# Performance work log

Measured on AMD Instinct MI355X. Metric: run time of the kernel, lower is better.

Reference implementation:

```python
import jax, jax.numpy as jnp
import numpy as np

N, E, IN, HID, H, G, OUT = 50000, 800000, 128, 96, 8, 64, 10
D = HID // H  # per-head dim = 12


def setup_inputs() -> dict:
    key = jax.random.key(0)
    ks = jax.random.split(key, 24)
    s = 0.1
    inp = {
        'x': jax.random.normal(ks[0], (N, IN), jnp.float32),
        'src': jax.random.randint(ks[1], (E,), 0, N, jnp.int32),
        'dst': jax.random.randint(ks[2], (E,), 0, N, jnp.int32),
        'graph_id': jax.random.randint(ks[3], (N,), 0, G, jnp.int32),
        # GraphConv layers (norm='both', weight + bias)
        'W1': jax.random.normal(ks[4], (IN, HID), jnp.float32) * s,
        'b1': jnp.zeros((HID,), jnp.float32),
        'W2': jax.random.normal(ks[5], (HID, HID), jnp.float32) * s,
        'b2': jnp.zeros((HID,), jnp.float32),
        # 3 GATv2 layers, stacked params
        'Ws': jax.random.normal(ks[6], (3, HID, HID), jnp.float32) * s,
        'bs': jnp.zeros((3, HID), jnp.float32),
        'Wd': jax.random.normal(ks[7], (3, HID, HID), jnp.float32) * s,
        'bd': jnp.zeros((3, HID), jnp.float32),
        'attn': jax.random.normal(ks[8], (3, H, D), jnp.float32) * s,
        # classifier MLP (dropout is identity at inference)
        'Wc1': jax.random.normal(ks[9], (HID, HID), jnp.float32) * s,
        'bc1': jnp.zeros((HID,), jnp.float32),
        'Wc2': jax.random.normal(ks[10], (HID, HID // 2), jnp.float32) * s,
        'bc2': jnp.zeros((HID // 2,), jnp.float32),
        'Wc3': jax.random.normal(ks[11], (HID // 2, OUT), jnp.float32) * s,
        'bc3': jnp.zeros((OUT,), jnp.float32),
    }
    return inp


def _graph_conv(h, W, b, src, dst):
    # DGL GraphConv, norm='both', allow_zero_in_degree (degrees clamped to >=1)
    ones = jnp.ones((E,), h.dtype)
    deg_out = jnp.clip(jax.ops.segment_sum(ones, src, N), 1.0)
    deg_in = jnp.clip(jax.ops.segment_sum(ones, dst, N), 1.0)
    h = (h * (deg_out ** -0.5)[:, None]) @ W          # [N, out]
    agg = jax.ops.segment_sum(h[src], dst, N)          # sum over in-edges
    return agg * (deg_in ** -0.5)[:, None] + b


def _gatv2(h, Ws, bs, Wd, bd, attn, src, dst):
    fs = (h @ Ws + bs).reshape(N, H, D)
    fd = (h @ Wd + bd).reshape(N, H, D)
    e = jax.nn.leaky_relu(fs[src] + fd[dst], 0.2)      # [E, H, D]
    logits = jnp.einsum('ehd,hd->eh', e, attn)         # [E, H]
    # edge softmax over incoming edges of each dst node
    m = jax.ops.segment_max(logits, dst, N)            # [N, H]
    ex = jnp.exp(logits - m[dst])
    den = jax.ops.segment_sum(ex, dst, N)              # [N, H]
    a = ex / den[dst]                                  # [E, H]
    rst = jax.ops.segment_sum(a[:, :, None] * fs[src], dst, N)  # [N, H, D]
    return jax.nn.relu(rst).reshape(N, HID)            # activation=relu, then view


def reference(x, src, dst, graph_id, W1, b1, W2, b2, Ws, bs, Wd, bd, attn,
              Wc1, bc1, Wc2, bc2, Wc3, bc3):
    h = jax.nn.relu(_graph_conv(x, W1, b1, src, dst))
    h = jax.nn.relu(_graph_conv(h, W2, b2, src, dst))
    for i in range(3):
        h = _gatv2(h, Ws[i], bs[i], Wd[i], bd[i], attn[i], src, dst)
    # dgl.max_nodes: per-graph max readout
    hg = jax.ops.segment_max(h, graph_id, G)           # [G, HID]
    z = jax.nn.relu(hg @ Wc1 + bc1)
    z = jax.nn.relu(z @ Wc2 + bc2)
    return z @ Wc3 + bc3                               # [G, OUT]
```

## Files before the change

### kernel.cpp

```cpp
#include <hip/hip_runtime.h>
#include <hip/hip_bf16.h>

#define Nn 50000
#define Ee 800000
#define INF_ 128
#define HIDF 96
#define HH 8
#define DD 12
#define GG 64
#define OUTF 10

#define SCAN_CHUNK 512
#define SCAN_BLOCKS ((Nn + SCAN_CHUNK - 1) / SCAN_CHUNK)
#define RB 128

__global__ void hist_kernel(const int* __restrict__ src, const int* __restrict__ dst,
                            int* cnt_out, int* cnt_in, int* __restrict__ edge_slot, int E) {
    int e = blockIdx.x * 256 + threadIdx.x;
    if (e < E) {
        atomicAdd(&cnt_out[src[e]], 1);
        edge_slot[e] = atomicAdd(&cnt_in[dst[e]], 1);
    }
}

__global__ __launch_bounds__(256) void scan1_kernel(const int* __restrict__ cnt_in,
                                                    int* __restrict__ row_start,
                                                    int* __restrict__ blk_sum, int N) {
    __shared__ int part[256];
    int t = threadIdx.x;
    int base = blockIdx.x * SCAN_CHUNK;
    int i0 = base + 2 * t, i1 = i0 + 1;
    int a = (i0 < N) ? cnt_in[i0] : 0;
    int b = (i1 < N) ? cnt_in[i1] : 0;
    int s = a + b;
    part[t] = s;
    __syncthreads();
    for (int off = 1; off < 256; off <<= 1) {
        int v = (t >= off) ? part[t - off] : 0;
        __syncthreads();
        part[t] += v;
        __syncthreads();
    }
    int excl = part[t] - s;
    if (i0 < N) row_start[i0] = excl;
    if (i1 < N) row_start[i1] = excl + a;
    if (t == 255) blk_sum[blockIdx.x] = part[255];
}

__global__ __launch_bounds__(128) void scan2_kernel(const int* __restrict__ blk_sum,
                                                    int* __restrict__ blk_off,
                                                    int* __restrict__ row_start, int N) {
    __shared__ int part[128];
    int t = threadIdx.x;
    int v0 = (t < SCAN_BLOCKS) ? blk_sum[t] : 0;
    part[t] = v0;
    __syncthreads();
    for (int off = 1; off < 128; off <<= 1) {
        int v = (t >= off) ? part[t - off] : 0;
        __syncthreads();
        part[t] += v;
        __syncthreads();
    }
    blk_off[t] = part[t] - v0;
    if (t == 127) row_start[N] = part[127];
}

__global__ __launch_bounds__(256) void scan3_kernel(int* __restrict__ row_start,
                                                    const int* __restrict__ blk_off, int N) {
    int t = threadIdx.x;
    int base = blockIdx.x * SCAN_CHUNK;
    int off = blk_off[blockIdx.x];
    int i0 = base + 2 * t, i1 = i0 + 1;
    if (i0 < N) row_start[i0] += off;
    if (i1 < N) row_start[i1] += off;
}

__global__ void node_setup(const int* __restrict__ cnt_in, const int* __restrict__ cnt_out,
                           float* __restrict__ degI_is, float* __restrict__ degO_is, int N) {
    int n = blockIdx.x * 256 + threadIdx.x;
    if (n < N) {
        degI_is[n] = rsqrtf((float)max(cnt_in[n], 1));
        degO_is[n] = rsqrtf((float)max(cnt_out[n], 1));
    }
}

__global__ void fill_kernel(const int* __restrict__ src, const int* __restrict__ dst,
                            const int* __restrict__ row_start, const int* __restrict__ edge_slot,
                            int* __restrict__ csr_src, int E) {
    int e = blockIdx.x * 256 + threadIdx.x;
    if (e < E) {
        csr_src[row_start[dst[e]] + edge_slot[e]] = src[e];
    }
}

__global__ __launch_bounds__(192) void gemm96(const float* __restrict__ A, int K,
                                              const float* __restrict__ W,
                                              const float* __restrict__ bias,
                                              const float* __restrict__ rowScale,
                                              float* __restrict__ out, int N) {
    __shared__ float A_lds[64 * 36];
    __shared__ float W_lds[32 * 96];
    const int t = threadIdx.x;
    const int row0 = blockIdx.x * 64;
    const int tcol = t % 24;
    const int trow = t / 24;
    float acc[8][4];
#pragma unroll
    for (int i = 0; i < 8; ++i)
#pragma unroll
        for (int j = 0; j < 4; ++j) acc[i][j] = 0.f;

    for (int k0 = 0; k0 < K; k0 += 32) {
        for (int i = t; i < 32 * 24; i += 192) {
            ((float4*)W_lds)[i] = ((const float4*)W)[(size_t)k0 * 24 + i];
        }
        for (int i = t; i < 64 * 8; i += 192) {
            int r = i / 8, kk = i % 8;
            int gr = row0 + r;
            float4 v = make_float4(0.f, 0.f, 0.f, 0.f);
            if (gr < N) {
                v = *((const float4*)(A + (size_t)gr * K + k0 + kk * 4));
                if (rowScale) {
                    float s = rowScale[gr];
                    v.x *= s; v.y *= s; v.z *= s; v.w *= s;
                }
            }
            *((float4*)(A_lds + r * 36 + kk * 4)) = v;
        }
        __syncthreads();
#pragma unroll
        for (int kk4 = 0; kk4 < 8; ++kk4) {
            float4 a[8];
#pragma unroll
            for (int i = 0; i < 8; ++i)
                a[i] = *((const float4*)(A_lds + (trow + 8 * i) * 36 + kk4 * 4));
#pragma unroll
            for (int kk = 0; kk < 4; ++kk) {
                float4 wv = *((const float4*)(W_lds + (kk4 * 4 + kk) * 96 + tcol * 4));
#pragma unroll
                for (int i = 0; i < 8; ++i) {
                    float av = (kk == 0) ? a[i].x : (kk == 1) ? a[i].y : (kk == 2) ? a[i].z : a[i].w;
                    acc[i][0] = fmaf(av, wv.x, acc[i][0]);
                    acc[i][1] = fmaf(av, wv.y, acc[i][1]);
                    acc[i][2] = fmaf(av, wv.z, acc[i][2]);
                    acc[i][3] = fmaf(av, wv.w, acc[i][3]);
                }
            }
        }
        __syncthreads();
    }
    float4 b4 = bias ? *((const float4*)(bias + tcol * 4)) : make_float4(0.f, 0.f, 0.f, 0.f);
#pragma unroll
    for (int i = 0; i < 8; ++i) {
        int gr = row0 + trow + 8 * i;
        if (gr < N) {
            float4 o = make_float4(acc[i][0] + b4.x, acc[i][1] + b4.y,
                                   acc[i][2] + b4.z, acc[i][3] + b4.w);
            *((float4*)(out + (size_t)gr * 96 + tcol * 4)) = o;
        }
    }
}

__global__ __launch_bounds__(192) void gemm96x2(const float* __restrict__ A,
                                                const float* __restrict__ W1_, const float* __restrict__ b1_,
                                                const float* __restrict__ W2_, const float* __restrict__ b2_,
                                                float* __restrict__ out1, float* __restrict__ out2, int N) {
    __shared__ float A_lds[64 * 36];
    __shared__ float W_lds[2 * 32 * 96];
    const int t = threadIdx.x;
    const int row0 = blockIdx.x * 64;
    const int tcol = t % 24;
    const int trow = t / 24;
    float acc1[8][4], acc2[8][4];
#pragma unroll
    for (int i = 0; i < 8; ++i)
#pragma unroll
        for (int j = 0; j < 4; ++j) { acc1[i][j] = 0.f; acc2[i][j] = 0.f; }

    for (int k0 = 0; k0 < 96; k0 += 32) {
        for (int i = t; i < 32 * 24; i += 192) {
            ((float4*)W_lds)[i] = ((const float4*)W1_)[(size_t)k0 * 24 + i];
            ((float4*)(W_lds + 32 * 96))[i] = ((const float4*)W2_)[(size_t)k0 * 24 + i];
        }
        for (int i = t; i < 64 * 8; i += 192) {
            int r = i / 8, kk = i % 8;
            int gr = row0 + r;
            float4 v = make_float4(0.f, 0.f, 0.f, 0.f);
            if (gr < N) v = *((const float4*)(A + (size_t)gr * 96 + k0 + kk * 4));
            *((float4*)(A_lds + r * 36 + kk * 4)) = v;
        }
        __syncthreads();
#pragma unroll
        for (int kk4 = 0; kk4 < 8; ++kk4) {
            float4 a[8];
#pragma unroll
            for (int i = 0; i < 8; ++i)
                a[i] = *((const float4*)(A_lds + (trow + 8 * i) * 36 + kk4 * 4));
#pragma unroll
            for (int kk = 0; kk < 4; ++kk) {
                float4 wv1 = *((const float4*)(W_lds + (kk4 * 4 + kk) * 96 + tcol * 4));
                float4 wv2 = *((const float4*)(W_lds + 32 * 96 + (kk4 * 4 + kk) * 96 + tcol * 4));
#pragma unroll
                for (int i = 0; i < 8; ++i) {
                    float av = (kk == 0) ? a[i].x : (kk == 1) ? a[i].y : (kk == 2) ? a[i].z : a[i].w;
                    acc1[i][0] = fmaf(av, wv1.x, acc1[i][0]);
                    acc1[i][1] = fmaf(av, wv1.y, acc1[i][1]);
                    acc1[i][2] = fmaf(av, wv1.z, acc1[i][2]);
                    acc1[i][3] = fmaf(av, wv1.w, acc1[i][3]);
                    acc2[i][0] = fmaf(av, wv2.x, acc2[i][0]);
                    acc2[i][1] = fmaf(av, wv2.y, acc2[i][1]);
                    acc2[i][2] = fmaf(av, wv2.z, acc2[i][2]);
                    acc2[i][3] = fmaf(av, wv2.w, acc2[i][3]);
                }
            }
        }
        __syncthreads();
    }
    float4 bb1 = *((const float4*)(b1_ + tcol * 4));
    float4 bb2 = *((const float4*)(b2_ + tcol * 4));
#pragma unroll
    for (int i = 0; i < 8; ++i) {
        int gr = row0 + trow + 8 * i;
        if (gr < N) {
            float4 o1 = make_float4(acc1[i][0] + bb1.x, acc1[i][1] + bb1.y,
                                    acc1[i][2] + bb1.z, acc1[i][3] + bb1.w);
            float4 o2 = make_float4(acc2[i][0] + bb2.x, acc2[i][1] + bb2.y,
                                    acc2[i][2] + bb2.z, acc2[i][3] + bb2.w);
            *((float4*)(out1 + (size_t)gr * 96 + tcol * 4)) = o1;
            *((float4*)(out2 + (size_t)gr * 96 + tcol * 4)) = o2;
        }
    }
}

__global__ __launch_bounds__(192) void gc_agg(const float* __restrict__ hW,
                                              const int* __restrict__ row_start,
                                              const int* __restrict__ csr_src,
                                              const float* __restrict__ degI_is,
                                              const float* __restrict__ bias,
                                              float* __restrict__ hout, int N) {
    int tid = blockIdx.x * 192 + threadIdx.x;
    int n = tid / 24;
    int c = (tid % 24) * 4;
    if (n >= N) return;
    int beg = row_start[n], end = row_start[n + 1];
    float4 s = make_float4(0.f, 0.f, 0.f, 0.f);
    int e = beg;
    for (; e + 4 <= end; e += 4) {
        int i0 = csr_src[e], i1 = csr_src[e + 1], i2 = csr_src[e + 2], i3 = csr_src[e + 3];
        float4 v0 = *(const float4*)(hW + (size_t)i0 * 96 + c);
        float4 v1 = *(const float4*)(hW + (size_t)i1 * 96 + c);
        float4 v2 = *(const float4*)(hW + (size_t)i2 * 96 + c);
        float4 v3 = *(const float4*)(hW + (size_t)i3 * 96 + c);
        s.x += (v0.x + v1.x) + (v2.x + v3.x);
        s.y += (v0.y + v1.y) + (v2.y + v3.y);
        s.z += (v0.z + v1.z) + (v2.z + v3.z);
        s.w += (v0.w + v1.w) + (v2.w + v3.w);
    }
    for (; e < end; ++e) {
        int i0 = csr_src[e];
        float4 v0 = *(const float4*)(hW + (size_t)i0 * 96 + c);
        s.x += v0.x; s.y += v0.y; s.z += v0.z; s.w += v0.w;
    }
    float dn = degI_is[n];
    float4 b = *(const float4*)(bias + c);
    float4 o;
    o.x = fmaxf(fmaf(s.x, dn, b.x), 0.f);
    o.y = fmaxf(fmaf(s.y, dn, b.y), 0.f);
    o.z = fmaxf(fmaf(s.z, dn, b.z), 0.f);
    o.w = fmaxf(fmaf(s.w, dn, b.w), 0.f);
    *(float4*)(hout + (size_t)n * 96 + c) = o;
}

__global__ __launch_bounds__(256) void gat_agg(const float* __restrict__ fs,
                                               const float* __restrict__ fd,
                                               const float* __restrict__ attn,
                                               const int* __restrict__ row_start,
                                               const int* __restrict__ csr_src,
                                               float* __restrict__ hout, int N) {
    int tid = blockIdx.x * 256 + threadIdx.x;
    int n = tid >> 3, hd = tid & 7;
    if (n >= N) return;
    float att[12], fdv[12];
    {
        const float4* ap = (const float4*)(attn + hd * 12);
        float4 a0 = ap[0], a1 = ap[1], a2 = ap[2];
        att[0]=a0.x; att[1]=a0.y; att[2]=a0.z; att[3]=a0.w;
        att[4]=a1.x; att[5]=a1.y; att[6]=a1.z; att[7]=a1.w;
        att[8]=a2.x; att[9]=a2.y; att[10]=a2.z; att[11]=a2.w;
        const float4* dp = (const float4*)(fd + (size_t)n * 96 + hd * 12);
        float4 d0 = dp[0], d1 = dp[1], d2 = dp[2];
        fdv[0]=d0.x; fdv[1]=d0.y; fdv[2]=d0.z; fdv[3]=d0.w;
        fdv[4]=d1.x; fdv[5]=d1.y; fdv[6]=d1.z; fdv[7]=d1.w;
        fdv[8]=d2.x; fdv[9]=d2.y; fdv[10]=d2.z; fdv[11]=d2.w;
    }
    int beg = row_start[n], end = row_start[n + 1];
    float m = -3.0e38f, den = 0.f;
    float acc[12];
#pragma unroll
    for (int d = 0; d < 12; ++d) acc[d] = 0.f;

    auto process = [&](const float4& s0, const float4& s1, const float4& s2) {
        float fsv[12];
        fsv[0]=s0.x; fsv[1]=s0.y; fsv[2]=s0.z; fsv[3]=s0.w;
        fsv[4]=s1.x; fsv[5]=s1.y; fsv[6]=s1.z; fsv[7]=s1.w;
        fsv[8]=s2.x; fsv[9]=s2.y; fsv[10]=s2.z; fsv[11]=s2.w;
        float logit = 0.f;
#pragma unroll
        for (int d = 0; d < 12; ++d) {
            float u = fsv[d] + fdv[d];
            u = u > 0.f ? u : 0.2f * u;
            logit = fmaf(u, att[d], logit);
        }
        float nm = fmaxf(m, logit);
        float cc = __expf(m - nm);
        float w  = __expf(logit - nm);
        den = fmaf(den, cc, w);
#pragma unroll
        for (int d = 0; d < 12; ++d) acc[d] = fmaf(acc[d], cc, w * fsv[d]);
        m = nm;
    };

    int e = beg;
    for (; e + 4 <= end; e += 4) {
        int i0 = csr_src[e], i1 = csr_src[e + 1], i2 = csr_src[e + 2], i3 = csr_src[e + 3];
        const float4* p0 = (const float4*)(fs + (size_t)i0 * 96 + hd * 12);
        const float4* p1 = (const float4*)(fs + (size_t)i1 * 96 + hd * 12);
        const float4* p2 = (const float4*)(fs + (size_t)i2 * 96 + hd * 12);
        const float4* p3 = (const float4*)(fs + (size_t)i3 * 96 + hd * 12);
        float4 a0 = p0[0], a1 = p0[1], a2 = p0[2];
        float4 b0 = p1[0], b1 = p1[1], b2 = p1[2];
        float4 c0 = p2[0], c1 = p2[1], c2 = p2[2];
        float4 d0 = p3[0], d1 = p3[1], d2 = p3[2];
        process(a0, a1, a2);
        process(b0, b1, b2);
        process(c0, c1, c2);
        process(d0, d1, d2);
    }
    for (; e < end; ++e) {
        int i0 = csr_src[e];
        const float4* p0 = (const float4*)(fs + (size_t)i0 * 96 + hd * 12);
        float4 a0 = p0[0], a1 = p0[1], a2 = p0[2];
        process(a0, a1, a2);
    }
    float inv = den > 0.f ? 1.f / den : 0.f;
    float* op = hout + (size_t)n * 96 + hd * 12;
#pragma unroll
    for (int d = 0; d < 12; ++d) op[d] = fmaxf(acc[d] * inv, 0.f);
}

__global__ __launch_bounds__(384) void readout_partial(const float* __restrict__ h,
                                                       const int* __restrict__ graph_id,
                                                       float* __restrict__ partial, int N) {
    __shared__ int lhg[GG * 96];
    int t = threadIdx.x;
    for (int i = t; i < GG * 96; i += 384) lhg[i] = 0;
    __syncthreads();
    int f = t % 96, nl = t / 96;
    for (int n0 = blockIdx.x * 4; n0 < N; n0 += RB * 4) {
        int n = n0 + nl;
        if (n < N) {
            int g = graph_id[n];
            float v = h[(size_t)n * 96 + f];
            atomicMax(&lhg[g * 96 + f], __float_as_int(v));
        }
    }
    __syncthreads();
    for (int i = t; i < GG * 96; i += 384)
        partial[(size_t)blockIdx.x * (GG * 96) + i] = __int_as_float(lhg[i]);
}

__global__ void readout_reduce(const float* __restrict__ partial, float* __restrict__ hg) {
    int i = blockIdx.x * 256 + threadIdx.x;
    if (i < GG * 96) {
        float m = 0.f;
        for (int b = 0; b < RB; ++b) m = fmaxf(m, partial[(size_t)b * (GG * 96) + i]);
        hg[i] = m;
    }
}

__global__ __launch_bounds__(96) void mlp_kernel(const float* __restrict__ hg,
                                                 const float* __restrict__ Wc1, const float* __restrict__ bc1,
                                                 const float* __restrict__ Wc2, const float* __restrict__ bc2,
                                                 const float* __restrict__ Wc3, const float* __restrict__ bc3,
                                                 float* __restrict__ out) {
    int g = blockIdx.x;
    int t = threadIdx.x;
    __shared__ float z0[96], z1[96], z2[48];
    z0[t] = hg[(size_t)g * 96 + t];
    __syncthreads();
    float s = bc1[t];
    for (int k = 0; k < 96; ++k) s = fmaf(z0[k], Wc1[k * 96 + t], s);
    z1[t] = fmaxf(s, 0.f);
    __syncthreads();
    if (t < 48) {
        float s2 = bc2[t];
        for (int k = 0; k < 96; ++k) s2 = fmaf(z1[k], Wc2[k * 48 + t], s2);
        z2[t] = fmaxf(s2, 0.f);
    }
    __syncthreads();
    if (t < 10) {
        float s3 = bc3[t];
        for (int k = 0; k < 48; ++k) s3 = fmaf(z2[k], Wc3[k * 10 + t], s3);
        out[(size_t)g * 10 + t] = s3;
    }
}

extern "C" void kernel_launch(void* const* d_in, const int* in_sizes, int n_in,
                              void* d_out, int out_size, void* d_ws, size_t ws_size,
                              hipStream_t stream) {
    const float* x        = (const float*)d_in[0];
    const int*   src      = (const int*)d_in[1];
    const int*   dst      = (const int*)d_in[2];
    const int*   graph_id = (const int*)d_in[3];
    const float* W1  = (const float*)d_in[4];
    const float* b1  = (const float*)d_in[5];
    const float* W2  = (const float*)d_in[6];
    const float* b2  = (const float*)d_in[7];
    const float* Ws  = (const float*)d_in[8];
    const float* bs  = (const float*)d_in[9];
    const float* Wd  = (const float*)d_in[10];
    const float* bd  = (const float*)d_in[11];
    const float* attn = (const float*)d_in[12];
    const float* Wc1 = (const float*)d_in[13];
    const float* bc1 = (const float*)d_in[14];
    const float* Wc2 = (const float*)d_in[15];
    const float* bc2 = (const float*)d_in[16];
    const float* Wc3 = (const float*)d_in[17];
    const float* bc3 = (const float*)d_in[18];
    float* out = (float*)d_out;

    char* ws = (char*)d_ws;
    size_t off = 0;
    auto alloc = [&](size_t bytes) {
        char* p = ws + off;
        off = (off + bytes + 255) & ~(size_t)255;
        return p;
    };
    int*   cnt_in    = (int*)alloc(Nn * 4);
    int*   cnt_out   = (int*)alloc(Nn * 4);
    int*   row_start = (int*)alloc((Nn + 1) * 4);
    int*   edge_slot = (int*)alloc(Ee * 4);
    int*   csr_src   = (int*)alloc(Ee * 4);
    float* degI_is   = (float*)alloc(Nn * 4);
    float* degO_is   = (float*)alloc(Nn * 4);
    float* bufH      = (float*)alloc((size_t)Nn * 96 * 4);
    float* bufT      = (float*)alloc((size_t)Nn * 96 * 4);
    float* bufFd     = (float*)alloc((size_t)Nn * 96 * 4);
    float* hg        = (float*)alloc(GG * 96 * 4);
    float* partial   = (float*)alloc((size_t)RB * GG * 96 * 4);
    int*   blk_sum   = (int*)alloc(128 * 4);
    int*   blk_off   = (int*)alloc(128 * 4);

    hipMemsetAsync(cnt_in, 0, Nn * 4, stream);
    hipMemsetAsync(cnt_out, 0, Nn * 4, stream);

    int eb = (Ee + 255) / 256;
    hist_kernel<<<eb, 256, 0, stream>>>(src, dst, cnt_out, cnt_in, edge_slot, Ee);
    scan1_kernel<<<SCAN_BLOCKS, 256, 0, stream>>>(cnt_in, row_start, blk_sum, Nn);
    scan2_kernel<<<1, 128, 0, stream>>>(blk_sum, blk_off, row_start, Nn);
    scan3_kernel<<<SCAN_BLOCKS, 256, 0, stream>>>(row_start, blk_off, Nn);
    node_setup<<<(Nn + 255) / 256, 256, 0, stream>>>(cnt_in, cnt_out, degI_is, degO_is, Nn);
    fill_kernel<<<eb, 256, 0, stream>>>(src, dst, row_start, edge_slot, csr_src, Ee);

    int gemm_blocks = (Nn + 63) / 64;
    int agg_blocks  = (Nn * 24 + 191) / 192;
    int gat_blocks  = (Nn * 8 + 255) / 256;

    gemm96<<<gemm_blocks, 192, 0, stream>>>(x, 128, W1, nullptr, degO_is, bufT, Nn);
    gc_agg<<<agg_blocks, 192, 0, stream>>>(bufT, row_start, csr_src, degI_is, b1, bufH, Nn);
    gemm96<<<gemm_blocks, 192, 0, stream>>>(bufH, 96, W2, nullptr, degO_is, bufT, Nn);
    gc_agg<<<agg_blocks, 192, 0, stream>>>(bufT, row_start, csr_src, degI_is, b2, bufH, Nn);

    for (int l = 0; l < 3; ++l) {
        const float* Wsl = Ws + (size_t)l * 96 * 96;
        const float* bsl = bs + (size_t)l * 96;
        const float* Wdl = Wd + (size_t)l * 96 * 96;
        const float* bdl = bd + (size_t)l * 96;
        const float* atl = attn + (size_t)l * 96;
        gemm96x2<<<gemm_blocks, 192, 0, stream>>>(bufH, Wsl, bsl, Wdl, bdl, bufT, bufFd, Nn);
        gat_agg<<<gat_blocks, 256, 0, stream>>>(bufT, bufFd, atl, row_start, csr_src, bufH, Nn);
    }

    readout_partial<<<RB, 384, 0, stream>>>(bufH, graph_id, partial, Nn);
    readout_reduce<<<(GG * 96 + 255) / 256, 256, 0, stream>>>(partial, hg);
    mlp_kernel<<<GG, 96, 0, stream>>>(hg, Wc1, bc1, Wc2, bc2, Wc3, bc3, out);
}
```

Baseline: 679.1 us.

## Build CSR with range-partitioned LDS histograms instead of global atomics

Replaces the global-atomic histogram and scatter fill with a two-level scheme. Node IDs are split into 8 ranges, and each block counts one edge chunk into LDS histograms. A per-range column scan then produces chunk offsets, and a fill kernel scatters edges using LDS cursors. This removes contended global atomics and the edge_slot array. In exchange, every range block rereads all of src and dst (8x edge reads), and the partial buffers are placed in the bufT and bufFd scratch space.

```diff
diff --git a/kernel.cpp b/kernel.cpp
--- a/kernel.cpp
+++ b/kernel.cpp
@@ -14,12 +14,76 @@
 #define SCAN_BLOCKS ((Nn + SCAN_CHUNK - 1) / SCAN_CHUNK)
 #define RB 128
 
-__global__ void hist_kernel(const int* __restrict__ src, const int* __restrict__ dst,
-                            int* cnt_out, int* cnt_in, int* __restrict__ edge_slot, int E) {
-    int e = blockIdx.x * 256 + threadIdx.x;
-    if (e < E) {
-        atomicAdd(&cnt_out[src[e]], 1);
-        edge_slot[e] = atomicAdd(&cnt_in[dst[e]], 1);
+#define RNG 8
+#define RBINS 6256
+#define CHK 32
+#define CHKE (Ee / CHK)
+
+__global__ __launch_bounds__(256) void csr_hist(const int* __restrict__ src,
+                                                const int* __restrict__ dst,
+                                                int* __restrict__ partS,
+                                                int* __restrict__ partD) {
+    __shared__ int hS[RBINS], hD[RBINS];
+    int r = blockIdx.x / CHK, b = blockIdx.x % CHK;
+    int t = threadIdx.x;
+    for (int i = t; i < RBINS; i += 256) { hS[i] = 0; hD[i] = 0; }
+    __syncthreads();
+    int lo = r * RBINS;
+    int base = b * CHKE;
+    for (int i = t; i < CHKE; i += 256) {
+        int s = src[base + i] - lo;
+        if ((unsigned)s < RBINS) atomicAdd(&hS[s], 1);
+        int d = dst[base + i] - lo;
+        if ((unsigned)d < RBINS) atomicAdd(&hD[d], 1);
+    }
+    __syncthreads();
+    size_t po = ((size_t)r * CHK + b) * RBINS;
+    for (int i = t; i < RBINS; i += 256) {
+        partS[po + i] = hS[i];
+        partD[po + i] = hD[i];
+    }
+}
+
+__global__ void csr_scanchunks(int* __restrict__ partS, int* __restrict__ partD,
+                               int* __restrict__ cnt_in, int* __restrict__ cnt_out) {
+    int k = blockIdx.x * 256 + threadIdx.x;
+    if (k >= RNG * RBINS) return;
+    int r = k / RBINS, lb = k % RBINS;
+    size_t basep = (size_t)r * CHK * RBINS + lb;
+    int sumD = 0, sumS = 0;
+    for (int b = 0; b < CHK; ++b) {
+        size_t idx = basep + (size_t)b * RBINS;
+        int v = partD[idx];
+        partD[idx] = sumD;
+        sumD += v;
+        sumS += partS[idx];
+    }
+    if (k < Nn) { cnt_in[k] = sumD; cnt_out[k] = sumS; }
+}
+
+__global__ __launch_bounds__(256) void csr_fill(const int* __restrict__ src,
+                                                const int* __restrict__ dst,
+                                                const int* __restrict__ row_start,
+                                                const int* __restrict__ partD,
+                                                int* __restrict__ csr_src) {
+    __shared__ int cur[RBINS];
+    int r = blockIdx.x / CHK, b = blockIdx.x % CHK;
+    int t = threadIdx.x;
+    size_t po = ((size_t)r * CHK + b) * RBINS;
+    int lo = r * RBINS;
+    for (int i = t; i < RBINS; i += 256) {
+        int node = lo + i;
+        int rs = (node < Nn) ? row_start[node] : 0;
+        cur[i] = rs + partD[po + i];
+    }
+    __syncthreads();
+    int base = b * CHKE;
+    for (int i = t; i < CHKE; i += 256) {
+        int d = dst[base + i] - lo;
+        if ((unsigned)d < RBINS) {
+            int slot = atomicAdd(&cur[d], 1);
+            csr_src[slot] = src[base + i];
+        }
     }
 }
 
@@ -81,15 +145,6 @@
     if (n < N) {
         degI_is[n] = rsqrtf((float)max(cnt_in[n], 1));
         degO_is[n] = rsqrtf((float)max(cnt_out[n], 1));
-    }
-}
-
-__global__ void fill_kernel(const int* __restrict__ src, const int* __restrict__ dst,
-                            const int* __restrict__ row_start, const int* __restrict__ edge_slot,
-                            int* __restrict__ csr_src, int E) {
-    int e = blockIdx.x * 256 + threadIdx.x;
-    if (e < E) {
-        csr_src[row_start[dst[e]] + edge_slot[e]] = src[e];
     }
 }
 
@@ -439,7 +494,6 @@
     int*   cnt_in    = (int*)alloc(Nn * 4);
     int*   cnt_out   = (int*)alloc(Nn * 4);
     int*   row_start = (int*)alloc((Nn + 1) * 4);
-    int*   edge_slot = (int*)alloc(Ee * 4);
     int*   csr_src   = (int*)alloc(Ee * 4);
     float* degI_is   = (float*)alloc(Nn * 4);
     float* degO_is   = (float*)alloc(Nn * 4);
@@ -451,16 +505,16 @@
     int*   blk_sum   = (int*)alloc(128 * 4);
     int*   blk_off   = (int*)alloc(128 * 4);
 
-    hipMemsetAsync(cnt_in, 0, Nn * 4, stream);
-    hipMemsetAsync(cnt_out, 0, Nn * 4, stream);
-
-    int eb = (Ee + 255) / 256;
-    hist_kernel<<<eb, 256, 0, stream>>>(src, dst, cnt_out, cnt_in, edge_slot, Ee);
+    int* partS = (int*)bufT;
+    int* partD = (int*)bufFd;
+
+    csr_hist<<<RNG * CHK, 256, 0, stream>>>(src, dst, partS, partD);
+    csr_scanchunks<<<(RNG * RBINS + 255) / 256, 256, 0, stream>>>(partS, partD, cnt_in, cnt_out);
     scan1_kernel<<<SCAN_BLOCKS, 256, 0, stream>>>(cnt_in, row_start, blk_sum, Nn);
     scan2_kernel<<<1, 128, 0, stream>>>(blk_sum, blk_off, row_start, Nn);
     scan3_kernel<<<SCAN_BLOCKS, 256, 0, stream>>>(row_start, blk_off, Nn);
     node_setup<<<(Nn + 255) / 256, 256, 0, stream>>>(cnt_in, cnt_out, degI_is, degO_is, Nn);
-    fill_kernel<<<eb, 256, 0, stream>>>(src, dst, row_start, edge_slot, csr_src, Ee);
+    csr_fill<<<RNG * CHK, 256, 0, stream>>>(src, dst, row_start, partD, csr_src);
 
     int gemm_blocks = (Nn + 63) / 64;
     int agg_blocks  = (Nn * 24 + 191) / 192;
```

New measurement: 704.1 us. 3.7% more time.

## Build degrees with LDS-packed histograms and process nodes in degree-sorted order

Applied to the files above, without the earlier changes.

Degree counting moves from global atomics to per-block LDS histograms with four 8-bit counters packed per word, followed by a reduction kernel. CSR fill now claims slots with an atomic cursor, which removes the edge_slot array. A counting sort by in-degree builds a node permutation that the GraphConv and GATv2 aggregation kernels use, so lanes in a wavefront handle nodes of similar degree and diverge less. The risks are overflow of the 8-bit counters if any node's degree exceeds 255, scattered output writes in the aggregation kernels, and a few extra small launches.

```diff
diff --git a/kernel.cpp b/kernel.cpp
--- a/kernel.cpp
+++ b/kernel.cpp
@@ -14,12 +14,52 @@
 #define SCAN_BLOCKS ((Nn + SCAN_CHUNK - 1) / SCAN_CHUNK)
 #define RB 128
 
-__global__ void hist_kernel(const int* __restrict__ src, const int* __restrict__ dst,
-                            int* cnt_out, int* cnt_in, int* __restrict__ edge_slot, int E) {
-    int e = blockIdx.x * 256 + threadIdx.x;
-    if (e < E) {
-        atomicAdd(&cnt_out[src[e]], 1);
-        edge_slot[e] = atomicAdd(&cnt_in[dst[e]], 1);
+#define HCHK 256
+#define HCHKE (Ee / HCHK)
+#define NW 12512
+#define DBIN 64
+
+__global__ __launch_bounds__(256) void hist_lds(const int* __restrict__ src,
+                                                const int* __restrict__ dst,
+                                                unsigned int* __restrict__ partS,
+                                                unsigned int* __restrict__ partD) {
+    __shared__ unsigned int h[NW];
+    int b = blockIdx.x, t = threadIdx.x;
+    for (int i = t; i < NW; i += 256) h[i] = 0u;
+    __syncthreads();
+    int base = b * HCHKE;
+    for (int i = t; i < HCHKE; i += 256) {
+        int d = dst[base + i];
+        atomicAdd(&h[d >> 2], 1u << ((d & 3) * 8));
+    }
+    __syncthreads();
+    for (int i = t; i < NW; i += 256) { partD[(size_t)b * NW + i] = h[i]; h[i] = 0u; }
+    __syncthreads();
+    for (int i = t; i < HCHKE; i += 256) {
+        int s = src[base + i];
+        atomicAdd(&h[s >> 2], 1u << ((s & 3) * 8));
+    }
+    __syncthreads();
+    for (int i = t; i < NW; i += 256) partS[(size_t)b * NW + i] = h[i];
+}
+
+__global__ void hist_reduce(const unsigned int* __restrict__ partS,
+                            const unsigned int* __restrict__ partD,
+                            int* __restrict__ cnt_in, int* __restrict__ cnt_out) {
+    int w = blockIdx.x * 256 + threadIdx.x;
+    if (w >= NW) return;
+    unsigned int totS = 0u, totD = 0u;
+    for (int b = 0; b < HCHK; ++b) {
+        totS += partS[(size_t)b * NW + w];
+        totD += partD[(size_t)b * NW + w];
+    }
+#pragma unroll
+    for (int j = 0; j < 4; ++j) {
+        int k = w * 4 + j;
+        if (k < Nn) {
+            cnt_in[k]  = (int)((totD >> (j * 8)) & 0xFFu);
+            cnt_out[k] = (int)((totS >> (j * 8)) & 0xFFu);
+        }
     }
 }
 
@@ -76,21 +116,71 @@
 }
 
 __global__ void node_setup(const int* __restrict__ cnt_in, const int* __restrict__ cnt_out,
+                           const int* __restrict__ row_start, int* __restrict__ cursor,
                            float* __restrict__ degI_is, float* __restrict__ degO_is, int N) {
     int n = blockIdx.x * 256 + threadIdx.x;
     if (n < N) {
+        cursor[n] = row_start[n];
         degI_is[n] = rsqrtf((float)max(cnt_in[n], 1));
         degO_is[n] = rsqrtf((float)max(cnt_out[n], 1));
     }
 }
 
 __global__ void fill_kernel(const int* __restrict__ src, const int* __restrict__ dst,
-                            const int* __restrict__ row_start, const int* __restrict__ edge_slot,
-                            int* __restrict__ csr_src, int E) {
+                            int* __restrict__ cursor, int* __restrict__ csr_src, int E) {
     int e = blockIdx.x * 256 + threadIdx.x;
     if (e < E) {
-        csr_src[row_start[dst[e]] + edge_slot[e]] = src[e];
-    }
+        int slot = atomicAdd(&cursor[dst[e]], 1);
+        csr_src[slot] = src[e];
+    }
+}
+
+__global__ __launch_bounds__(256) void deg_hist(const int* __restrict__ cnt_in,
+                                                int* __restrict__ dcnt, int N) {
+    __shared__ int h[DBIN];
+    int t = threadIdx.x;
+    if (t < DBIN) h[t] = 0;
+    __syncthreads();
+    int n = blockIdx.x * 256 + t;
+    if (n < N) atomicAdd(&h[min(cnt_in[n], DBIN - 1)], 1);
+    __syncthreads();
+    if (t < DBIN && h[t]) atomicAdd(&dcnt[t], h[t]);
+}
+
+__global__ __launch_bounds__(64) void deg_scan(const int* __restrict__ dcnt,
+                                               int* __restrict__ dcur) {
+    __shared__ int p[DBIN];
+    int t = threadIdx.x;
+    int v0 = dcnt[t];
+    p[t] = v0;
+    __syncthreads();
+    for (int o = 1; o < DBIN; o <<= 1) {
+        int v = (t >= o) ? p[t - o] : 0;
+        __syncthreads();
+        p[t] += v;
+        __syncthreads();
+    }
+    dcur[t] = p[t] - v0;
+}
+
+__global__ __launch_bounds__(256) void perm_fill(const int* __restrict__ cnt_in,
+                                                 int* __restrict__ dcur,
+                                                 int* __restrict__ perm, int N) {
+    __shared__ int lh[DBIN];
+    __shared__ int lbase[DBIN];
+    int t = threadIdx.x;
+    if (t < DBIN) lh[t] = 0;
+    __syncthreads();
+    int n = blockIdx.x * 256 + t;
+    int bin = 0, lslot = 0;
+    if (n < N) {
+        bin = min(cnt_in[n], DBIN - 1);
+        lslot = atomicAdd(&lh[bin], 1);
+    }
+    __syncthreads();
+    if (t < DBIN) lbase[t] = lh[t] ? atomicAdd(&dcur[t], lh[t]) : 0;
+    __syncthreads();
+    if (n < N) perm[lbase[bin] + lslot] = n;
 }
 
 __global__ __launch_bounds__(192) void gemm96(const float* __restrict__ A, int K,
@@ -237,11 +327,13 @@
                                               const int* __restrict__ csr_src,
                                               const float* __restrict__ degI_is,
                                               const float* __restrict__ bias,
+                                              const int* __restrict__ perm,
                                               float* __restrict__ hout, int N) {
     int tid = blockIdx.x * 192 + threadIdx.x;
-    int n = tid / 24;
+    int p = tid / 24;
     int c = (tid % 24) * 4;
-    if (n >= N) return;
+    if (p >= N) return;
+    int n = perm[p];
     int beg = row_start[n], end = row_start[n + 1];
     float4 s = make_float4(0.f, 0.f, 0.f, 0.f);
     int e = beg;
@@ -276,10 +368,12 @@
                                                const float* __restrict__ attn,
                                                const int* __restrict__ row_start,
                                                const int* __restrict__ csr_src,
+                                               const int* __restrict__ perm,
                                                float* __restrict__ hout, int N) {
     int tid = blockIdx.x * 256 + threadIdx.x;
-    int n = tid >> 3, hd = tid & 7;
-    if (n >= N) return;
+    int p = tid >> 3, hd = tid & 7;
+    if (p >= N) return;
+    int n = perm[p];
     float att[12], fdv[12];
     {
         const float4* ap = (const float4*)(attn + hd * 12);
@@ -439,8 +533,9 @@
     int*   cnt_in    = (int*)alloc(Nn * 4);
     int*   cnt_out   = (int*)alloc(Nn * 4);
     int*   row_start = (int*)alloc((Nn + 1) * 4);
-    int*   edge_slot = (int*)alloc(Ee * 4);
+    int*   cursor    = (int*)alloc(Nn * 4);
     int*   csr_src   = (int*)alloc(Ee * 4);
+    int*   perm      = (int*)alloc(Nn * 4);
     float* degI_is   = (float*)alloc(Nn * 4);
     float* degO_is   = (float*)alloc(Nn * 4);
     float* bufH      = (float*)alloc((size_t)Nn * 96 * 4);
@@ -450,26 +545,35 @@
     float* partial   = (float*)alloc((size_t)RB * GG * 96 * 4);
     int*   blk_sum   = (int*)alloc(128 * 4);
     int*   blk_off   = (int*)alloc(128 * 4);
-
-    hipMemsetAsync(cnt_in, 0, Nn * 4, stream);
-    hipMemsetAsync(cnt_out, 0, Nn * 4, stream);
-
-    int eb = (Ee + 255) / 256;
-    hist_kernel<<<eb, 256, 0, stream>>>(src, dst, cnt_out, cnt_in, edge_slot, Ee);
+    int*   dcnt      = (int*)alloc(DBIN * 4);
+    int*   dcur      = (int*)alloc(DBIN * 4);
+
+    unsigned int* partS = (unsigned int*)bufT;
+    unsigned int* partD = (unsigned int*)bufFd;
+
+    hipMemsetAsync(dcnt, 0, DBIN * 4, stream);
+
+    hist_lds<<<HCHK, 256, 0, stream>>>(src, dst, partS, partD);
+    hist_reduce<<<(NW + 255) / 256, 256, 0, stream>>>(partS, partD, cnt_in, cnt_out);
     scan1_kernel<<<SCAN_BLOCKS, 256, 0, stream>>>(cnt_in, row_start, blk_sum, Nn);
     scan2_kernel<<<1, 128, 0, stream>>>(blk_sum, blk_off, row_start, Nn);
     scan3_kernel<<<SCAN_BLOCKS, 256, 0, stream>>>(row_start, blk_off, Nn);
-    node_setup<<<(Nn + 255) / 256, 256, 0, stream>>>(cnt_in, cnt_out, degI_is, degO_is, Nn);
-    fill_kernel<<<eb, 256, 0, stream>>>(src, dst, row_start, edge_slot, csr_src, Ee);
+    node_setup<<<(Nn + 255) / 256, 256, 0, stream>>>(cnt_in, cnt_out, row_start, cursor,
+                                                     degI_is, degO_is, Nn);
+    fill_kernel<<<(Ee + 255) / 256, 256, 0, stream>>>(src, dst, cursor, csr_src, Ee);
+
+    deg_hist<<<(Nn + 255) / 256, 256, 0, stream>>>(cnt_in, dcnt, Nn);
+    deg_scan<<<1, 64, 0, stream>>>(dcnt, dcur);
+    perm_fill<<<(Nn + 255) / 256, 256, 0, stream>>>(cnt_in, dcur, perm, Nn);
 
     int gemm_blocks = (Nn + 63) / 64;
     int agg_blocks  = (Nn * 24 + 191) / 192;
     int gat_blocks  = (Nn * 8 + 255) / 256;
 
     gemm96<<<gemm_blocks, 192, 0, stream>>>(x, 128, W1, nullptr, degO_is, bufT, Nn);
-    gc_agg<<<agg_blocks, 192, 0, stream>>>(bufT, row_start, csr_src, degI_is, b1, bufH, Nn);
+    gc_agg<<<agg_blocks, 192, 0, stream>>>(bufT, row_start, csr_src, degI_is, b1, perm, bufH, Nn);
     gemm96<<<gemm_blocks, 192, 0, stream>>>(bufH, 96, W2, nullptr, degO_is, bufT, Nn);
-    gc_agg<<<agg_blocks, 192, 0, stream>>>(bufT, row_start, csr_src, degI_is, b2, bufH, Nn);
+    gc_agg<<<agg_blocks, 192, 0, stream>>>(bufT, row_start, csr_src, degI_is, b2, perm, bufH, Nn);
 
     for (int l = 0; l < 3; ++l) {
         const float* Wsl = Ws + (size_t)l * 96 * 96;
@@ -478,7 +582,7 @@
         const float* bdl = bd + (size_t)l * 96;
         const float* atl = attn + (size_t)l * 96;
         gemm96x2<<<gemm_blocks, 192, 0, stream>>>(bufH, Wsl, bsl, Wdl, bdl, bufT, bufFd, Nn);
-        gat_agg<<<gat_blocks, 256, 0, stream>>>(bufT, bufFd, atl, row_start, csr_src, bufH, Nn);
+        gat_agg<<<gat_blocks, 256, 0, stream>>>(bufT, bufFd, atl, row_start, csr_src, perm, bufH, Nn);
     }
 
     readout_partial<<<RB, 384, 0, stream>>>(bufH, graph_id, partial, Nn);
```

Result: no change. 676.4 us (-0.4%).
